# Performance work log

Hardware: AMD Instinct MI355X
Metric: run time of the kernel (lower is better)

Reference implementation:

```python
import jax, jax.numpy as jnp
import numpy as np
import math

EMB = 128
N_HEADS = 8
HEAD_DIM = EMB // N_HEADS
TANH_CLIP = 10.0
NEG_INF = -1e9


def make_heads(x, n_heads):
    # x: (B, n, H) -> (B, n_heads, n, head_dim)
    B, n, H = x.shape
    return x.reshape(B, n, n_heads, H // n_heads).transpose(0, 2, 1, 3)


def setup_inputs() -> dict:
    key = jax.random.key(0)
    ks = jax.random.split(key, 11)
    B, N, H = 64, 2000, EMB
    s = 1.0 / math.sqrt(H)
    return {
        "patch_embeddings": jax.random.normal(ks[0], (B, N, H), jnp.float32),
        "fixed_content_cls": jax.random.normal(ks[1], (B, 1, H), jnp.float32),
        "Wq_graph": jax.random.normal(ks[2], (H, H), jnp.float32) * s,
        "Wq_first": jax.random.normal(ks[3], (H, H), jnp.float32) * s,
        "Wq_last": jax.random.normal(ks[4], (H, H), jnp.float32) * s,
        "Wk": jax.random.normal(ks[5], (H, H), jnp.float32) * s,
        "Wv": jax.random.normal(ks[6], (H, H), jnp.float32) * s,
        "logit_Wk": jax.random.normal(ks[7], (H, H), jnp.float32) * s,
        "Wc": jax.random.normal(ks[8], (H, H), jnp.float32) * s,
        "bc": jax.random.normal(ks[9], (H,), jnp.float32) * s,
        "last_patch": jax.random.randint(ks[10], (B,), 0, N, jnp.int64),
    }


def reference(patch_embeddings, fixed_content_cls, Wq_graph, Wq_first, Wq_last,
              Wk, Wv, logit_Wk, Wc, bc, last_patch):
    B, N, H = patch_embeddings.shape
    bidx = jnp.arange(B)

    # reset(): precomputed projections over all patches (memory-dominant)
    q_graph = make_heads(fixed_content_cls @ Wq_graph.T, N_HEADS)   # (B, nh, 1, hd)
    glimpse_k = make_heads(patch_embeddings @ Wk.T, N_HEADS)        # (B, nh, N, hd)
    glimpse_v = make_heads(patch_embeddings @ Wv.T, N_HEADS)        # (B, nh, N, hd)
    logit_k = patch_embeddings @ logit_Wk.T                          # (B, N, H)

    # mask the just-visited patch (emulate -inf with large negative for stability)
    mask = jnp.zeros((B, N), patch_embeddings.dtype).at[bidx, last_patch].set(NEG_INF)

    # gather last patch embedding: (B, 1, H)
    last_emb = patch_embeddings[bidx, last_patch][:, None, :]
    q_first = make_heads(last_emb @ Wq_first.T, N_HEADS)
    q_last = make_heads(last_emb @ Wq_last.T, N_HEADS)
    glimpse_q = q_graph + q_first + q_last                          # (B, nh, 1, hd)

    # masked multi-head attention, q_len = 1
    scores = jnp.einsum('bhqd,bhnd->bhqn', glimpse_q, glimpse_k) / math.sqrt(HEAD_DIM)
    scores = scores + mask[:, None, None, :]
    attn = jax.nn.softmax(scores, axis=-1)
    out = jnp.einsum('bhqn,bhnd->bhqd', attn, glimpse_v)            # (B, nh, 1, hd)
    out = out.transpose(0, 2, 1, 3).reshape(B, 1, H)

    final_q = out @ Wc.T + bc                                        # (B, 1, H)

    # tanh-clipped pointer logits over all N patches
    score = jnp.einsum('bqh,bnh->bqn', final_q, logit_k) / math.sqrt(H)  # (B, 1, N)
    score_masked = TANH_CLIP * jnp.tanh(score[:, 0, :]) + mask          # (B, N)
    probs = jax.nn.softmax(score_masked, axis=1)
    return probs
```

## Files before the change

kernel.cpp:

```cpp
#include <hip/hip_runtime.h>
#include <math.h>

#define BB 64
#define NN 2000
#define HH 128
#define NHEAD 8

__global__ __launch_bounds__(128) void k1_prep(
    const float* __restrict__ pe, const float* __restrict__ cls,
    const float* __restrict__ Wqg, const float* __restrict__ Wqf,
    const float* __restrict__ Wql, const float* __restrict__ Wk,
    const int* __restrict__ lp, float* __restrict__ qk_out) {
  __shared__ float sc[HH], sl[HH], q[HH];
  int b = blockIdx.x, t = threadIdx.x;
  int last = lp[b];
  sc[t] = cls[b*HH + t];
  sl[t] = pe[((long)b*NN + last)*HH + t];
  __syncthreads();
  float acc = 0.f;
  for (int j = 0; j < HH; j++)
    acc += Wqg[t*HH+j]*sc[j] + (Wqf[t*HH+j] + Wql[t*HH+j])*sl[j];
  q[t] = acc;
  __syncthreads();
  for (int h = 0; h < NHEAD; h++) {
    float a = 0.f;
    for (int d = 0; d < 16; d++)
      a += q[h*16+d] * Wk[(h*16+d)*HH + t];
    qk_out[(b*NHEAD + h)*HH + t] = a * 0.25f;
  }
}

__global__ __launch_bounds__(256) void k2_attn(
    const float* __restrict__ pe, const float* __restrict__ qk,
    const int* __restrict__ lp, float* __restrict__ lout, float* __restrict__ Wout,
    int splits, int rpb) {
  int b = blockIdx.y, sp = blockIdx.x, tid = threadIdx.x;
  __shared__ float4 smem4[1032];
  float4* qks4  = smem4;
  float4* plds4 = smem4 + 256;
  float*  smem  = (float*)smem4;

  const float4* qkg = (const float4*)(qk + b*NHEAD*HH);
  if (tid < 256) qks4[tid] = qkg[tid];
  __syncthreads();

  int last = lp[b];
  int r0 = sp * rpb;
  int r1 = min(r0 + rpb, NN);
  int r = tid >> 3, o = tid & 7;
  int w = tid >> 6, lane = tid & 63;

  float wacc[NHEAD][2];
  float lacc[NHEAD];
  #pragma unroll
  for (int h = 0; h < NHEAD; h++) { wacc[h][0]=0.f; wacc[h][1]=0.f; lacc[h]=0.f; }

  const float4* peg = (const float4*)pe;

  for (int base = r0; base < r1; base += 64) {
    int nA = base + r;
    int nB = base + 32 + r;
    bool vA = nA < r1, vB = nB < r1;
    long offA = (long)(b*NN + (vA ? nA : r1-1)) * 32;
    long offB = (long)(b*NN + (vB ? nB : r1-1)) * 32;
    float4 a4[4], b4[4];
    #pragma unroll
    for (int t = 0; t < 4; t++) {
      a4[t] = peg[offA + o + 8*t];
      b4[t] = peg[offB + o + 8*t];
    }
    float sA[NHEAD], sB[NHEAD];
    #pragma unroll
    for (int h = 0; h < NHEAD; h++) {
      float accA = 0.f, accB = 0.f;
      #pragma unroll
      for (int t = 0; t < 4; t++) {
        float4 k4 = qks4[h*32 + o + 8*t];
        accA += a4[t].x*k4.x + a4[t].y*k4.y + a4[t].z*k4.z + a4[t].w*k4.w;
        accB += b4[t].x*k4.x + b4[t].y*k4.y + b4[t].z*k4.z + b4[t].w*k4.w;
      }
      sA[h] = accA; sB[h] = accB;
    }
    #pragma unroll
    for (int h = 0; h < NHEAD; h++) {
      #pragma unroll
      for (int d = 1; d < 8; d <<= 1) {
        sA[h] += __shfl_xor(sA[h], d);
        sB[h] += __shfl_xor(sB[h], d);
      }
    }
    bool mA = vA && (nA != last), mB = vB && (nB != last);
    if (o == 0) {
      float4 pa0, pa1, pb0, pb1;
      pa0.x = mA ? __expf(sA[0]) : 0.f; pa0.y = mA ? __expf(sA[1]) : 0.f;
      pa0.z = mA ? __expf(sA[2]) : 0.f; pa0.w = mA ? __expf(sA[3]) : 0.f;
      pa1.x = mA ? __expf(sA[4]) : 0.f; pa1.y = mA ? __expf(sA[5]) : 0.f;
      pa1.z = mA ? __expf(sA[6]) : 0.f; pa1.w = mA ? __expf(sA[7]) : 0.f;
      pb0.x = mB ? __expf(sB[0]) : 0.f; pb0.y = mB ? __expf(sB[1]) : 0.f;
      pb0.z = mB ? __expf(sB[2]) : 0.f; pb0.w = mB ? __expf(sB[3]) : 0.f;
      pb1.x = mB ? __expf(sB[4]) : 0.f; pb1.y = mB ? __expf(sB[5]) : 0.f;
      pb1.z = mB ? __expf(sB[6]) : 0.f; pb1.w = mB ? __expf(sB[7]) : 0.f;
      plds4[r*2+0] = pa0; plds4[r*2+1] = pa1;
      plds4[(32+r)*2+0] = pb0; plds4[(32+r)*2+1] = pb1;
    }
    __syncthreads();

    #pragma unroll 4
    for (int i = 0; i < 16; i++) {
      int s = w*8 + (i&7) + ((i>>3)<<5);
      int n = base + s;
      long off = (long)(b*NN + min(n, NN-1)) * HH;
      float v0 = pe[off + lane];
      float v1 = pe[off + 64 + lane];
      float4 plo = plds4[s*2], phi = plds4[s*2+1];
      float pl[NHEAD] = {plo.x, plo.y, plo.z, plo.w, phi.x, phi.y, phi.z, phi.w};
      #pragma unroll
      for (int h = 0; h < NHEAD; h++) {
        wacc[h][0] += pl[h]*v0;
        wacc[h][1] += pl[h]*v1;
        lacc[h]    += pl[h];
      }
    }
    __syncthreads();
  }

  #pragma unroll
  for (int h = 0; h < NHEAD; h++) {
    smem[w*1024 + h*HH + lane]      = wacc[h][0];
    smem[w*1024 + h*HH + 64 + lane] = wacc[h][1];
  }
  if (lane == 0) {
    #pragma unroll
    for (int h = 0; h < NHEAD; h++) smem[4096 + w*NHEAD + h] = lacc[h];
  }
  __syncthreads();
  int h2 = tid >> 5, j4 = tid & 31;
  float4 sum = smem4[h2*32 + j4];
  float4 s1 = smem4[256 + h2*32 + j4];
  float4 s2 = smem4[512 + h2*32 + j4];
  float4 s3 = smem4[768 + h2*32 + j4];
  sum.x += s1.x + s2.x + s3.x; sum.y += s1.y + s2.y + s3.y;
  sum.z += s1.z + s2.z + s3.z; sum.w += s1.w + s2.w + s3.w;
  float4* Wo = (float4*)(Wout + ((long)(b*splits + sp)*NHEAD + h2)*HH);
  Wo[j4] = sum;
  if (tid < NHEAD)
    lout[(b*splits + sp)*NHEAD + tid] =
        smem[4096+tid] + smem[4096+8+tid] + smem[4096+16+tid] + smem[4096+24+tid];
}

__global__ __launch_bounds__(128) void k3a(
    const float* __restrict__ lpart, const float* __restrict__ Wpart,
    float* __restrict__ Wn, int splits) {
  int b = blockIdx.x, h = blockIdx.y, t = threadIdx.x;
  float acc = 0.f, ls = 0.f;
  #pragma unroll 4
  for (int s = 0; s < splits; s++) {
    acc += Wpart[((long)(b*splits+s)*NHEAD + h)*HH + t];
    ls  += lpart[(b*splits+s)*NHEAD + h];
  }
  Wn[(b*NHEAD+h)*HH + t] = acc / ls;
}

__global__ __launch_bounds__(128) void k3b(
    const float* __restrict__ Wn, const float* __restrict__ Wv,
    const float* __restrict__ Wc, const float* __restrict__ bc,
    const float* __restrict__ lWk, float* __restrict__ lq_out) {
  int b = blockIdx.x, t = threadIdx.x;
  __shared__ float Wns[NHEAD*HH], outf[HH], fq[HH];
  for (int i = t; i < NHEAD*HH; i += 128) Wns[i] = Wn[b*NHEAD*HH + i];
  __syncthreads();
  {
    int h = t >> 4;
    float a = 0.f;
    for (int j = 0; j < HH; j++) a += Wv[t*HH+j] * Wns[h*HH+j];
    outf[t] = a;
  }
  __syncthreads();
  {
    float a = bc[t];
    for (int k = 0; k < HH; k++) a += Wc[t*HH+k] * outf[k];
    fq[t] = a;
  }
  __syncthreads();
  {
    float a = 0.f;
    for (int i = 0; i < HH; i++) a += fq[i] * lWk[i*HH+t];
    lq_out[b*HH+t] = a * 0.08838834764831845f;
  }
}

__global__ __launch_bounds__(256) void k4_logits(
    const float* __restrict__ pe, const float* __restrict__ lq,
    const int* __restrict__ lp, float* __restrict__ eout, float* __restrict__ psum,
    int splits4, int rpb4) {
  int b = blockIdx.y, sp = blockIdx.x, tid = threadIdx.x;
  __shared__ float4 lqs4[32];
  __shared__ float red[4];
  if (tid < 32) lqs4[tid] = ((const float4*)(lq + b*HH))[tid];
  __syncthreads();
  int last = lp[b];
  int r0 = sp*rpb4, r1 = min(r0+rpb4, NN);
  int r = tid>>3, o = tid&7;
  const float4* peg = (const float4*)pe;
  float mysum = 0.f;
  for (int base = r0; base < r1; base += 64) {
    int nA = base + r, nB = base + 32 + r;
    bool vA = nA < r1, vB = nB < r1;
    long offA = (long)(b*NN + (vA ? nA : r1-1)) * 32;
    long offB = (long)(b*NN + (vB ? nB : r1-1)) * 32;
    float4 a4[4], b4[4];
    #pragma unroll
    for (int t = 0; t < 4; t++) { a4[t] = peg[offA + o + 8*t]; b4[t] = peg[offB + o + 8*t]; }
    float accA = 0.f, accB = 0.f;
    #pragma unroll
    for (int t = 0; t < 4; t++) {
      float4 k4 = lqs4[o + 8*t];
      accA += a4[t].x*k4.x + a4[t].y*k4.y + a4[t].z*k4.z + a4[t].w*k4.w;
      accB += b4[t].x*k4.x + b4[t].y*k4.y + b4[t].z*k4.z + b4[t].w*k4.w;
    }
    #pragma unroll
    for (int d = 1; d < 8; d <<= 1) {
      accA += __shfl_xor(accA, d);
      accB += __shfl_xor(accB, d);
    }
    if (o == 0) {
      if (vA) {
        float e = (nA == last) ? 0.f : __expf(10.f*tanhf(accA) - 10.f);
        eout[b*NN + nA] = e;
        mysum += e;
      }
      if (vB) {
        float e = (nB == last) ? 0.f : __expf(10.f*tanhf(accB) - 10.f);
        eout[b*NN + nB] = e;
        mysum += e;
      }
    }
  }
  #pragma unroll
  for (int d = 1; d < 64; d <<= 1) mysum += __shfl_xor(mysum, d);
  int w = tid>>6;
  if ((tid&63) == 0) red[w] = mysum;
  __syncthreads();
  if (tid == 0) psum[b*splits4+sp] = red[0]+red[1]+red[2]+red[3];
}

__global__ __launch_bounds__(256) void k5_scale(
    const float* __restrict__ eout, const float* __restrict__ psum,
    float* __restrict__ out, int splits4) {
  int b = blockIdx.y, sp = blockIdx.x, tid = threadIdx.x;
  __shared__ float S;
  if (tid == 0) {
    float a = 0.f;
    for (int s = 0; s < splits4; s++) a += psum[b*splits4+s];
    S = a;
  }
  __syncthreads();
  float inv = 1.f / S;
  int per = (NN + gridDim.x - 1) / gridDim.x;
  int lo = sp*per, hi = min(lo+per, NN);
  for (int n = lo + tid; n < hi; n += 256)
    out[b*NN + n] = eout[b*NN + n] * inv;
}

extern "C" void kernel_launch(void* const* d_in, const int* in_sizes, int n_in,
                              void* d_out, int out_size, void* d_ws, size_t ws_size,
                              hipStream_t stream) {
  const float* pe   = (const float*)d_in[0];
  const float* cls  = (const float*)d_in[1];
  const float* Wqg  = (const float*)d_in[2];
  const float* Wqf  = (const float*)d_in[3];
  const float* Wql  = (const float*)d_in[4];
  const float* Wk   = (const float*)d_in[5];
  const float* Wv   = (const float*)d_in[6];
  const float* lWk  = (const float*)d_in[7];
  const float* Wc   = (const float*)d_in[8];
  const float* bc   = (const float*)d_in[9];
  const int*   lp   = (const int*)d_in[10];
  float* out = (float*)d_out;
  float* ws  = (float*)d_ws;

  int S2 = 32;
  {
    size_t need = (size_t)(65536 + BB*32*NHEAD + (size_t)BB*32*NHEAD*HH
                           + BB*NHEAD*HH + BB*HH + BB*NN + BB*32) * 4;
    if (ws_size < need) S2 = 8;
  }
  int rpb = (NN + S2 - 1) / S2;
  const int S4 = 32, rpb4 = (NN + S4 - 1) / S4;

  float* qk    = ws;
  float* lpart = qk + BB*NHEAD*HH;
  float* Wpart = lpart + BB*S2*NHEAD;
  float* Wn    = Wpart + (size_t)BB*S2*NHEAD*HH;
  float* lq    = Wn + BB*NHEAD*HH;
  float* eout  = lq + BB*HH;
  float* psum  = eout + BB*NN;

  k1_prep<<<dim3(BB), dim3(128), 0, stream>>>(pe, cls, Wqg, Wqf, Wql, Wk, lp, qk);
  k2_attn<<<dim3(S2, BB), dim3(256), 0, stream>>>(pe, qk, lp, lpart, Wpart, S2, rpb);
  k3a<<<dim3(BB, NHEAD), dim3(128), 0, stream>>>(lpart, Wpart, Wn, S2);
  k3b<<<dim3(BB), dim3(128), 0, stream>>>(Wn, Wv, Wc, bc, lWk, lq);
  k4_logits<<<dim3(S4, BB), dim3(256), 0, stream>>>(pe, lq, lp, eout, psum, S4, rpb4);
  k5_scale<<<dim3(8, BB), dim3(256), 0, stream>>>(eout, psum, out, S4);
}
```

Baseline: 66.70 us.

## Fuse attention score and value passes, merge combine kernels, vectorize prep

```diff
diff --git a/kernel.cpp b/kernel.cpp
--- a/kernel.cpp
+++ b/kernel.cpp
@@ -5,25 +5,39 @@
 #define NN 2000
 #define HH 128
 #define NHEAD 8
+#define S2 16
+#define S4 32
 
 __global__ __launch_bounds__(128) void k1_prep(
     const float* __restrict__ pe, const float* __restrict__ cls,
     const float* __restrict__ Wqg, const float* __restrict__ Wqf,
     const float* __restrict__ Wql, const float* __restrict__ Wk,
     const int* __restrict__ lp, float* __restrict__ qk_out) {
-  __shared__ float sc[HH], sl[HH], q[HH];
+  __shared__ float4 sc4[32], sl4[32];
+  __shared__ float q[HH];
   int b = blockIdx.x, t = threadIdx.x;
   int last = lp[b];
-  sc[t] = cls[b*HH + t];
-  sl[t] = pe[((long)b*NN + last)*HH + t];
-  __syncthreads();
+  if (t < 32) {
+    sc4[t] = ((const float4*)(cls + b*HH))[t];
+    sl4[t] = ((const float4*)(pe + ((long)b*NN + last)*HH))[t];
+  }
+  __syncthreads();
+  const float4* wg = (const float4*)(Wqg + t*HH);
+  const float4* wf = (const float4*)(Wqf + t*HH);
+  const float4* wl = (const float4*)(Wql + t*HH);
   float acc = 0.f;
-  for (int j = 0; j < HH; j++)
-    acc += Wqg[t*HH+j]*sc[j] + (Wqf[t*HH+j] + Wql[t*HH+j])*sl[j];
+  #pragma unroll 8
+  for (int j = 0; j < 32; j++) {
+    float4 g = wg[j], f = wf[j], l = wl[j], c = sc4[j], s = sl4[j];
+    acc += g.x*c.x + g.y*c.y + g.z*c.z + g.w*c.w;
+    acc += (f.x+l.x)*s.x + (f.y+l.y)*s.y + (f.z+l.z)*s.z + (f.w+l.w)*s.w;
+  }
   q[t] = acc;
   __syncthreads();
+  #pragma unroll
   for (int h = 0; h < NHEAD; h++) {
     float a = 0.f;
+    #pragma unroll
     for (int d = 0; d < 16; d++)
       a += q[h*16+d] * Wk[(h*16+d)*HH + t];
     qk_out[(b*NHEAD + h)*HH + t] = a * 0.25f;
@@ -33,174 +47,198 @@
 __global__ __launch_bounds__(256) void k2_attn(
     const float* __restrict__ pe, const float* __restrict__ qk,
     const int* __restrict__ lp, float* __restrict__ lout, float* __restrict__ Wout,
-    int splits, int rpb) {
+    int rpb) {
   int b = blockIdx.y, sp = blockIdx.x, tid = threadIdx.x;
-  __shared__ float4 smem4[1032];
-  float4* qks4  = smem4;
-  float4* plds4 = smem4 + 256;
-  float*  smem  = (float*)smem4;
-
-  const float4* qkg = (const float4*)(qk + b*NHEAD*HH);
-  if (tid < 256) qks4[tid] = qkg[tid];
-  __syncthreads();
+  int o = tid & 15, rr = tid >> 4;
+  int lane = tid & 63, w = tid >> 6;
+
+  const float4* qk4 = (const float4*)(qk + b*NHEAD*HH);
+  float4 qreg[NHEAD][2];
+  #pragma unroll
+  for (int h = 0; h < NHEAD; h++) {
+    qreg[h][0] = qk4[h*32 + o];
+    qreg[h][1] = qk4[h*32 + 16 + o];
+  }
 
   int last = lp[b];
-  int r0 = sp * rpb;
-  int r1 = min(r0 + rpb, NN);
-  int r = tid >> 3, o = tid & 7;
-  int w = tid >> 6, lane = tid & 63;
-
-  float wacc[NHEAD][2];
+  int r0 = sp * rpb, r1 = min(r0 + rpb, NN);
+  const float4* peg = (const float4*)pe;
+
+  float4 wacc[NHEAD][2];
   float lacc[NHEAD];
   #pragma unroll
-  for (int h = 0; h < NHEAD; h++) { wacc[h][0]=0.f; wacc[h][1]=0.f; lacc[h]=0.f; }
-
-  const float4* peg = (const float4*)pe;
-
-  for (int base = r0; base < r1; base += 64) {
-    int nA = base + r;
-    int nB = base + 32 + r;
+  for (int h = 0; h < NHEAD; h++) {
+    wacc[h][0] = make_float4(0.f,0.f,0.f,0.f);
+    wacc[h][1] = make_float4(0.f,0.f,0.f,0.f);
+    lacc[h] = 0.f;
+  }
+
+  for (int base = r0; base < r1; base += 32) {
+    int nA = base + rr, nB = base + 16 + rr;
     bool vA = nA < r1, vB = nB < r1;
     long offA = (long)(b*NN + (vA ? nA : r1-1)) * 32;
     long offB = (long)(b*NN + (vB ? nB : r1-1)) * 32;
-    float4 a4[4], b4[4];
-    #pragma unroll
-    for (int t = 0; t < 4; t++) {
-      a4[t] = peg[offA + o + 8*t];
-      b4[t] = peg[offB + o + 8*t];
-    }
+    float4 a0 = peg[offA + o],      a1 = peg[offA + 16 + o];
+    float4 b0 = peg[offB + o],      b1 = peg[offB + 16 + o];
     float sA[NHEAD], sB[NHEAD];
     #pragma unroll
     for (int h = 0; h < NHEAD; h++) {
-      float accA = 0.f, accB = 0.f;
-      #pragma unroll
-      for (int t = 0; t < 4; t++) {
-        float4 k4 = qks4[h*32 + o + 8*t];
-        accA += a4[t].x*k4.x + a4[t].y*k4.y + a4[t].z*k4.z + a4[t].w*k4.w;
-        accB += b4[t].x*k4.x + b4[t].y*k4.y + b4[t].z*k4.z + b4[t].w*k4.w;
-      }
-      sA[h] = accA; sB[h] = accB;
+      float4 q0 = qreg[h][0], q1 = qreg[h][1];
+      sA[h] = a0.x*q0.x + a0.y*q0.y + a0.z*q0.z + a0.w*q0.w
+            + a1.x*q1.x + a1.y*q1.y + a1.z*q1.z + a1.w*q1.w;
+      sB[h] = b0.x*q0.x + b0.y*q0.y + b0.z*q0.z + b0.w*q0.w
+            + b1.x*q1.x + b1.y*q1.y + b1.z*q1.z + b1.w*q1.w;
     }
     #pragma unroll
     for (int h = 0; h < NHEAD; h++) {
       #pragma unroll
-      for (int d = 1; d < 8; d <<= 1) {
+      for (int d = 1; d < 16; d <<= 1) {
         sA[h] += __shfl_xor(sA[h], d);
         sB[h] += __shfl_xor(sB[h], d);
       }
     }
     bool mA = vA && (nA != last), mB = vB && (nB != last);
-    if (o == 0) {
-      float4 pa0, pa1, pb0, pb1;
-      pa0.x = mA ? __expf(sA[0]) : 0.f; pa0.y = mA ? __expf(sA[1]) : 0.f;
-      pa0.z = mA ? __expf(sA[2]) : 0.f; pa0.w = mA ? __expf(sA[3]) : 0.f;
-      pa1.x = mA ? __expf(sA[4]) : 0.f; pa1.y = mA ? __expf(sA[5]) : 0.f;
-      pa1.z = mA ? __expf(sA[6]) : 0.f; pa1.w = mA ? __expf(sA[7]) : 0.f;
-      pb0.x = mB ? __expf(sB[0]) : 0.f; pb0.y = mB ? __expf(sB[1]) : 0.f;
-      pb0.z = mB ? __expf(sB[2]) : 0.f; pb0.w = mB ? __expf(sB[3]) : 0.f;
-      pb1.x = mB ? __expf(sB[4]) : 0.f; pb1.y = mB ? __expf(sB[5]) : 0.f;
-      pb1.z = mB ? __expf(sB[6]) : 0.f; pb1.w = mB ? __expf(sB[7]) : 0.f;
-      plds4[r*2+0] = pa0; plds4[r*2+1] = pa1;
-      plds4[(32+r)*2+0] = pb0; plds4[(32+r)*2+1] = pb1;
-    }
-    __syncthreads();
-
+    #pragma unroll
+    for (int h = 0; h < NHEAD; h++) {
+      float pA = mA ? __expf(sA[h]) : 0.f;
+      float pB = mB ? __expf(sB[h]) : 0.f;
+      wacc[h][0].x += pA*a0.x + pB*b0.x;
+      wacc[h][0].y += pA*a0.y + pB*b0.y;
+      wacc[h][0].z += pA*a0.z + pB*b0.z;
+      wacc[h][0].w += pA*a0.w + pB*b0.w;
+      wacc[h][1].x += pA*a1.x + pB*b1.x;
+      wacc[h][1].y += pA*a1.y + pB*b1.y;
+      wacc[h][1].z += pA*a1.z + pB*b1.z;
+      wacc[h][1].w += pA*a1.w + pB*b1.w;
+      lacc[h] += pA + pB;
+    }
+  }
+
+  #pragma unroll
+  for (int h = 0; h < NHEAD; h++) {
+    #pragma unroll
+    for (int t = 0; t < 2; t++) {
+      #pragma unroll
+      for (int d = 16; d < 64; d <<= 1) {
+        wacc[h][t].x += __shfl_xor(wacc[h][t].x, d);
+        wacc[h][t].y += __shfl_xor(wacc[h][t].y, d);
+        wacc[h][t].z += __shfl_xor(wacc[h][t].z, d);
+        wacc[h][t].w += __shfl_xor(wacc[h][t].w, d);
+      }
+    }
+    float v = lacc[h];
+    #pragma unroll
+    for (int d = 1; d < 64; d <<= 1) v += __shfl_xor(v, d);
+    lacc[h] = v;
+  }
+
+  __shared__ float4 red4[1024];
+  __shared__ float redl[32];
+  if (lane < 16) {
+    #pragma unroll
+    for (int h = 0; h < NHEAD; h++) {
+      red4[w*256 + lane*16 + h*2 + 0] = wacc[h][0];
+      red4[w*256 + lane*16 + h*2 + 1] = wacc[h][1];
+    }
+  }
+  if (lane == 0) {
+    #pragma unroll
+    for (int h = 0; h < NHEAD; h++) redl[w*NHEAD + h] = lacc[h];
+  }
+  __syncthreads();
+  {
+    int o2 = tid >> 4, h2 = (tid >> 1) & 7, t2 = tid & 1;
+    float4 s0 = red4[tid], s1 = red4[256 + tid], s2 = red4[512 + tid], s3 = red4[768 + tid];
+    float4 s;
+    s.x = s0.x + s1.x + s2.x + s3.x;
+    s.y = s0.y + s1.y + s2.y + s3.y;
+    s.z = s0.z + s1.z + s2.z + s3.z;
+    s.w = s0.w + s1.w + s2.w + s3.w;
+    float4* Wo = (float4*)(Wout + (long)(b*S2 + sp)*NHEAD*HH);
+    Wo[h2*32 + t2*16 + o2] = s;
+  }
+  if (tid < NHEAD)
+    lout[(b*S2 + sp)*NHEAD + tid] = redl[tid] + redl[8+tid] + redl[16+tid] + redl[24+tid];
+}
+
+__global__ __launch_bounds__(256) void k34(
+    const float* __restrict__ lpart, const float* __restrict__ Wpart,
+    const float* __restrict__ Wv, const float* __restrict__ Wc,
+    const float* __restrict__ bc, const float* __restrict__ lWk,
+    float* __restrict__ lq_out) {
+  int b = blockIdx.x, tid = threadIdx.x;
+  __shared__ float Wns[NHEAD*HH];
+  __shared__ float ls[NHEAD];
+  __shared__ float tmp[2][HH];
+  __shared__ float outf[HH], fq[HH];
+  for (int e = tid; e < NHEAD*HH; e += 256) {
+    float a = 0.f;
     #pragma unroll 4
-    for (int i = 0; i < 16; i++) {
-      int s = w*8 + (i&7) + ((i>>3)<<5);
-      int n = base + s;
-      long off = (long)(b*NN + min(n, NN-1)) * HH;
-      float v0 = pe[off + lane];
-      float v1 = pe[off + 64 + lane];
-      float4 plo = plds4[s*2], phi = plds4[s*2+1];
-      float pl[NHEAD] = {plo.x, plo.y, plo.z, plo.w, phi.x, phi.y, phi.z, phi.w};
-      #pragma unroll
-      for (int h = 0; h < NHEAD; h++) {
-        wacc[h][0] += pl[h]*v0;
-        wacc[h][1] += pl[h]*v1;
-        lacc[h]    += pl[h];
-      }
-    }
-    __syncthreads();
-  }
-
-  #pragma unroll
-  for (int h = 0; h < NHEAD; h++) {
-    smem[w*1024 + h*HH + lane]      = wacc[h][0];
-    smem[w*1024 + h*HH + 64 + lane] = wacc[h][1];
-  }
-  if (lane == 0) {
-    #pragma unroll
-    for (int h = 0; h < NHEAD; h++) smem[4096 + w*NHEAD + h] = lacc[h];
-  }
-  __syncthreads();
-  int h2 = tid >> 5, j4 = tid & 31;
-  float4 sum = smem4[h2*32 + j4];
-  float4 s1 = smem4[256 + h2*32 + j4];
-  float4 s2 = smem4[512 + h2*32 + j4];
-  float4 s3 = smem4[768 + h2*32 + j4];
-  sum.x += s1.x + s2.x + s3.x; sum.y += s1.y + s2.y + s3.y;
-  sum.z += s1.z + s2.z + s3.z; sum.w += s1.w + s2.w + s3.w;
-  float4* Wo = (float4*)(Wout + ((long)(b*splits + sp)*NHEAD + h2)*HH);
-  Wo[j4] = sum;
-  if (tid < NHEAD)
-    lout[(b*splits + sp)*NHEAD + tid] =
-        smem[4096+tid] + smem[4096+8+tid] + smem[4096+16+tid] + smem[4096+24+tid];
-}
-
-__global__ __launch_bounds__(128) void k3a(
-    const float* __restrict__ lpart, const float* __restrict__ Wpart,
-    float* __restrict__ Wn, int splits) {
-  int b = blockIdx.x, h = blockIdx.y, t = threadIdx.x;
-  float acc = 0.f, ls = 0.f;
-  #pragma unroll 4
-  for (int s = 0; s < splits; s++) {
-    acc += Wpart[((long)(b*splits+s)*NHEAD + h)*HH + t];
-    ls  += lpart[(b*splits+s)*NHEAD + h];
-  }
-  Wn[(b*NHEAD+h)*HH + t] = acc / ls;
-}
-
-__global__ __launch_bounds__(128) void k3b(
-    const float* __restrict__ Wn, const float* __restrict__ Wv,
-    const float* __restrict__ Wc, const float* __restrict__ bc,
-    const float* __restrict__ lWk, float* __restrict__ lq_out) {
-  int b = blockIdx.x, t = threadIdx.x;
-  __shared__ float Wns[NHEAD*HH], outf[HH], fq[HH];
-  for (int i = t; i < NHEAD*HH; i += 128) Wns[i] = Wn[b*NHEAD*HH + i];
-  __syncthreads();
+    for (int s = 0; s < S2; s++) a += Wpart[((long)(b*S2+s)*NHEAD)*HH + e];
+    Wns[e] = a;
+  }
+  if (tid < NHEAD) {
+    float l = 0.f;
+    for (int s = 0; s < S2; s++) l += lpart[(b*S2+s)*NHEAD + tid];
+    ls[tid] = l * (1.f/16.f);
+  }
+  __syncthreads();
+  int t = tid & 127, half = tid >> 7;
   {
     int h = t >> 4;
-    float a = 0.f;
-    for (int j = 0; j < HH; j++) a += Wv[t*HH+j] * Wns[h*HH+j];
-    outf[t] = a;
-  }
-  __syncthreads();
+    const float4* wv = (const float4*)(Wv + t*HH);
+    const float4* wn = (const float4*)(Wns + h*HH);
+    float a = 0.f;
+    #pragma unroll 4
+    for (int j = half*16; j < half*16 + 16; j++) {
+      float4 v = wv[j], n = wn[j];
+      a += v.x*n.x + v.y*n.y + v.z*n.z + v.w*n.w;
+    }
+    tmp[half][t] = a;
+    __syncthreads();
+    if (half == 0) outf[t] = (tmp[0][t] + tmp[1][t]) / ls[t>>4];
+    __syncthreads();
+  }
   {
-    float a = bc[t];
-    for (int k = 0; k < HH; k++) a += Wc[t*HH+k] * outf[k];
-    fq[t] = a;
-  }
-  __syncthreads();
+    const float4* wc = (const float4*)(Wc + t*HH);
+    const float4* of = (const float4*)outf;
+    float a = 0.f;
+    #pragma unroll 4
+    for (int k = half*16; k < half*16 + 16; k++) {
+      float4 v = wc[k], n = of[k];
+      a += v.x*n.x + v.y*n.y + v.z*n.z + v.w*n.w;
+    }
+    tmp[half][t] = a;
+    __syncthreads();
+    if (half == 0) fq[t] = tmp[0][t] + tmp[1][t] + bc[t];
+    __syncthreads();
+  }
   {
     float a = 0.f;
-    for (int i = 0; i < HH; i++) a += fq[i] * lWk[i*HH+t];
-    lq_out[b*HH+t] = a * 0.08838834764831845f;
+    #pragma unroll 4
+    for (int i = half*64; i < half*64 + 64; i++)
+      a += fq[i] * lWk[i*HH + t];
+    tmp[half][t] = a;
+    __syncthreads();
+    if (half == 0)
+      lq_out[b*HH + t] = (tmp[0][t] + tmp[1][t]) * 0.08838834764831845f;
   }
 }
 
 __global__ __launch_bounds__(256) void k4_logits(
     const float* __restrict__ pe, const float* __restrict__ lq,
     const int* __restrict__ lp, float* __restrict__ eout, float* __restrict__ psum,
-    int splits4, int rpb4) {
+    int rpb4) {
   int b = blockIdx.y, sp = blockIdx.x, tid = threadIdx.x;
-  __shared__ float4 lqs4[32];
+  int r = tid >> 3, o = tid & 7;
+  const float4* lq4 = (const float4*)(lq + b*HH);
+  float4 lreg[4];
+  #pragma unroll
+  for (int t = 0; t < 4; t++) lreg[t] = lq4[o + 8*t];
+
   __shared__ float red[4];
-  if (tid < 32) lqs4[tid] = ((const float4*)(lq + b*HH))[tid];
-  __syncthreads();
   int last = lp[b];
   int r0 = sp*rpb4, r1 = min(r0+rpb4, NN);
-  int r = tid>>3, o = tid&7;
   const float4* peg = (const float4*)pe;
   float mysum = 0.f;
   for (int base = r0; base < r1; base += 64) {
@@ -214,7 +252,7 @@
     float accA = 0.f, accB = 0.f;
     #pragma unroll
     for (int t = 0; t < 4; t++) {
-      float4 k4 = lqs4[o + 8*t];
+      float4 k4 = lreg[t];
       accA += a4[t].x*k4.x + a4[t].y*k4.y + a4[t].z*k4.z + a4[t].w*k4.w;
       accB += b4[t].x*k4.x + b4[t].y*k4.y + b4[t].z*k4.z + b4[t].w*k4.w;
     }
@@ -225,12 +263,12 @@
     }
     if (o == 0) {
       if (vA) {
-        float e = (nA == last) ? 0.f : __expf(10.f*tanhf(accA) - 10.f);
+        float e = (nA == last) ? 0.f : __expf(-20.f / (__expf(2.f*accA) + 1.f));
         eout[b*NN + nA] = e;
         mysum += e;
       }
       if (vB) {
-        float e = (nB == last) ? 0.f : __expf(10.f*tanhf(accB) - 10.f);
+        float e = (nB == last) ? 0.f : __expf(-20.f / (__expf(2.f*accB) + 1.f));
         eout[b*NN + nB] = e;
         mysum += e;
       }
@@ -238,26 +276,26 @@
   }
   #pragma unroll
   for (int d = 1; d < 64; d <<= 1) mysum += __shfl_xor(mysum, d);
-  int w = tid>>6;
-  if ((tid&63) == 0) red[w] = mysum;
-  __syncthreads();
-  if (tid == 0) psum[b*splits4+sp] = red[0]+red[1]+red[2]+red[3];
+  int w = tid >> 6;
+  if ((tid & 63) == 0) red[w] = mysum;
+  __syncthreads();
+  if (tid == 0) psum[b*S4 + sp] = red[0] + red[1] + red[2] + red[3];
 }
 
 __global__ __launch_bounds__(256) void k5_scale(
     const float* __restrict__ eout, const float* __restrict__ psum,
-    float* __restrict__ out, int splits4) {
+    float* __restrict__ out) {
   int b = blockIdx.y, sp = blockIdx.x, tid = threadIdx.x;
   __shared__ float S;
   if (tid == 0) {
     float a = 0.f;
-    for (int s = 0; s < splits4; s++) a += psum[b*splits4+s];
+    for (int s = 0; s < S4; s++) a += psum[b*S4 + s];
     S = a;
   }
   __syncthreads();
   float inv = 1.f / S;
   int per = (NN + gridDim.x - 1) / gridDim.x;
-  int lo = sp*per, hi = min(lo+per, NN);
+  int lo = sp*per, hi = min(lo + per, NN);
   for (int n = lo + tid; n < hi; n += 256)
     out[b*NN + n] = eout[b*NN + n] * inv;
 }
@@ -265,6 +303,7 @@
 extern "C" void kernel_launch(void* const* d_in, const int* in_sizes, int n_in,
                               void* d_out, int out_size, void* d_ws, size_t ws_size,
                               hipStream_t stream) {
+  (void)in_sizes; (void)n_in; (void)out_size; (void)ws_size;
   const float* pe   = (const float*)d_in[0];
   const float* cls  = (const float*)d_in[1];
   const float* Wqg  = (const float*)d_in[2];
@@ -279,27 +318,19 @@
   float* out = (float*)d_out;
   float* ws  = (float*)d_ws;
 
-  int S2 = 32;
-  {
-    size_t need = (size_t)(65536 + BB*32*NHEAD + (size_t)BB*32*NHEAD*HH
-                           + BB*NHEAD*HH + BB*HH + BB*NN + BB*32) * 4;
-    if (ws_size < need) S2 = 8;
-  }
-  int rpb = (NN + S2 - 1) / S2;
-  const int S4 = 32, rpb4 = (NN + S4 - 1) / S4;
+  const int rpb  = (NN + S2 - 1) / S2;
+  const int rpb4 = (NN + S4 - 1) / S4;
 
   float* qk    = ws;
   float* lpart = qk + BB*NHEAD*HH;
   float* Wpart = lpart + BB*S2*NHEAD;
-  float* Wn    = Wpart + (size_t)BB*S2*NHEAD*HH;
-  float* lq    = Wn + BB*NHEAD*HH;
+  float* lq    = Wpart + (size_t)BB*S2*NHEAD*HH;
   float* eout  = lq + BB*HH;
   float* psum  = eout + BB*NN;
 
   k1_prep<<<dim3(BB), dim3(128), 0, stream>>>(pe, cls, Wqg, Wqf, Wql, Wk, lp, qk);
-  k2_attn<<<dim3(S2, BB), dim3(256), 0, stream>>>(pe, qk, lp, lpart, Wpart, S2, rpb);
-  k3a<<<dim3(BB, NHEAD), dim3(128), 0, stream>>>(lpart, Wpart, Wn, S2);
-  k3b<<<dim3(BB), dim3(128), 0, stream>>>(Wn, Wv, Wc, bc, lWk, lq);
-  k4_logits<<<dim3(S4, BB), dim3(256), 0, stream>>>(pe, lq, lp, eout, psum, S4, rpb4);
-  k5_scale<<<dim3(8, BB), dim3(256), 0, stream>>>(eout, psum, out, S4);
-}
+  k2_attn<<<dim3(S2, BB), dim3(256), 0, stream>>>(pe, qk, lp, lpart, Wpart, rpb);
+  k34<<<dim3(BB), dim3(256), 0, stream>>>(lpart, Wpart, Wv, Wc, bc, lWk, lq);
+  k4_logits<<<dim3(S4, BB), dim3(256), 0, stream>>>(pe, lq, lp, eout, psum, rpb4);
+  k5_scale<<<dim3(8, BB), dim3(256), 0, stream>>>(eout, psum, out);
+}
```

After: 84.41 us. +26.6%, slower.
